# Kernel tuning notes

Hardware: AMD Instinct MI355X
Metric: run time of the kernel (lower is better)

## Reference

```python
import jax, jax.numpy as jnp
import numpy as np

D_K = 1024
D_V = 1024
D_IN = 1024
D_MODEL = 1024
NUM_HEADS = 16


def setup_inputs() -> dict:
    key = jax.random.key(0)
    k1, k2, k3, k4, k5 = jax.random.split(key, 5)
    x = jax.random.normal(k1, (4, 2048, D_IN), dtype=jnp.float32)
    # trunc_normal init approximated by clipped normal
    W_Q = jnp.clip(jax.random.normal(k2, (D_K, D_IN), dtype=jnp.float32), -2.0, 2.0)
    W_K = jnp.clip(jax.random.normal(k3, (D_K, D_IN), dtype=jnp.float32), -2.0, 2.0)
    W_V = jnp.clip(jax.random.normal(k4, (D_V, D_IN), dtype=jnp.float32), -2.0, 2.0)
    W_O = jnp.clip(jax.random.normal(k5, (D_MODEL, D_V), dtype=jnp.float32), -2.0, 2.0)
    return {"x": x, "W_Q": W_Q, "W_K": W_K, "W_V": W_V, "W_O": W_O}


def reference(x, W_Q, W_K, W_V, W_O):
    b, s, _ = x.shape
    h = NUM_HEADS
    hd_k = D_K // h
    hd_v = D_V // h
    wq = W_Q.reshape(h, hd_k, D_IN)
    wk = W_K.reshape(h, hd_k, D_IN)
    wv = W_V.reshape(h, hd_v, D_IN)
    # project: [b, h, s, head_dim]
    q = jnp.einsum('hkd,bsd->bhsk', wq, x)
    k = jnp.einsum('hkd,bsd->bhsk', wk, x)
    v = jnp.einsum('hvd,bsd->bhsv', wv, x)
    scale = 1.0 / jnp.sqrt(jnp.float32(hd_k))
    scores = jnp.einsum('bhnk,bhmk->bhnm', q, k) * scale  # [b,h,s,s]
    causal = jnp.tril(jnp.ones((s, s), dtype=bool))
    scores = jnp.where(causal, scores, -jnp.inf)
    attn = jax.nn.softmax(scores, axis=-1)
    out = jnp.einsum('bhnm,bhmv->bhnv', attn, v)  # [b,h,s,hd_v]
    out = out.transpose(0, 2, 1, 3).reshape(b, s, D_V)  # concat heads
    return jnp.einsum('ov,bsv->bso', W_O, out)
```

## Files before the change

kernel.cpp:

```cpp
#include <hip/hip_runtime.h>
#include <hip/hip_bf16.h>

typedef __bf16 bf16_t;
typedef __bf16 bf16x4 __attribute__((ext_vector_type(4)));
typedef __bf16 bf16x8 __attribute__((ext_vector_type(8)));
typedef float f32x4 __attribute__((ext_vector_type(4)));

#define MFMA16(a, b, c) __builtin_amdgcn_mfma_f32_16x16x32_bf16((a), (b), (c), 0, 0, 0)

#if __has_builtin(__builtin_amdgcn_exp2f)
#define EXP2(x) __builtin_amdgcn_exp2f(x)
#else
#define EXP2(x) exp2f(x)
#endif

__device__ inline void g2l16(const void* g, void* l) {
    __builtin_amdgcn_global_load_lds((const __attribute__((address_space(1))) void*)g,
                                     (__attribute__((address_space(3))) void*)l, 16, 0, 0);
}

__global__ __launch_bounds__(256) void cvt_split_k(const float* __restrict__ src,
                                                   bf16_t* __restrict__ hi,
                                                   bf16_t* __restrict__ lo, int n4) {
    int i = blockIdx.x * 256 + threadIdx.x;
    if (i < n4) {
        float4 v = reinterpret_cast<const float4*>(src)[i];
        bf16x4 h, l;
        float f;
        f = v.x; h[0] = (__bf16)f; l[0] = (__bf16)(f - (float)h[0]);
        f = v.y; h[1] = (__bf16)f; l[1] = (__bf16)(f - (float)h[1]);
        f = v.z; h[2] = (__bf16)f; l[2] = (__bf16)(f - (float)h[2]);
        f = v.w; h[3] = (__bf16)f; l[3] = (__bf16)(f - (float)h[3]);
        reinterpret_cast<bf16x4*>(hi)[i] = h;
        reinterpret_cast<bf16x4*>(lo)[i] = l;
    }
}

__global__ __launch_bounds__(256) void cvt_weights_k(const float* __restrict__ Wq,
                                                     const float* __restrict__ Wk,
                                                     const float* __restrict__ Wv,
                                                     const float* __restrict__ Wo,
                                                     bf16_t* __restrict__ WQKh, bf16_t* __restrict__ WQKl,
                                                     bf16_t* __restrict__ Wvh, bf16_t* __restrict__ Woh) {
    const int i = blockIdx.x * 256 + threadIdx.x;
    const int which = blockIdx.y;
    if (which <= 1) {
        const float c = (which == 0) ? 0.125f * 1.4426950408889634f : 1.0f;
        const int off = which * 262144;
        float4 v = reinterpret_cast<const float4*>(which == 0 ? Wq : Wk)[i];
        bf16x4 h, l;
        float f;
        f = v.x * c; h[0] = (__bf16)f; l[0] = (__bf16)(f - (float)h[0]);
        f = v.y * c; h[1] = (__bf16)f; l[1] = (__bf16)(f - (float)h[1]);
        f = v.z * c; h[2] = (__bf16)f; l[2] = (__bf16)(f - (float)h[2]);
        f = v.w * c; h[3] = (__bf16)f; l[3] = (__bf16)(f - (float)h[3]);
        reinterpret_cast<bf16x4*>(WQKh)[i + off] = h;
        reinterpret_cast<bf16x4*>(WQKl)[i + off] = l;
    } else {
        float4 v = reinterpret_cast<const float4*>(which == 2 ? Wv : Wo)[i];
        bf16x4 o;
        o[0] = (__bf16)v.x; o[1] = (__bf16)v.y; o[2] = (__bf16)v.z; o[3] = (__bf16)v.w;
        reinterpret_cast<bf16x4*>(which == 2 ? Wvh : Woh)[i] = o;
    }
}

template <int LGX>
__device__ inline void xcd_tile(int& bm, int& bn) {
    const int id = blockIdx.y * (1 << LGX) + blockIdx.x;
    const int cpx = ((1 << LGX) * gridDim.y) >> 3;
    const int swz = (id & 7) * cpx + (id >> 3);
    bn = swz & ((1 << LGX) - 1);
    bm = swz >> LGX;
}

template <int MODE>
__global__ __launch_bounds__(256) void gemm_bt(const bf16_t* __restrict__ A,
                                               const bf16_t* __restrict__ B,
                                               void* __restrict__ Cout,
                                               int M, int N, int K) {
    __shared__ __align__(16) bf16_t As[128 * 32];
    __shared__ __align__(16) bf16_t Bs[128 * 32];
    const int tid = threadIdx.x;
    const int w = tid >> 6, lane = tid & 63;
    const int l15 = lane & 15, g = lane >> 4;
    const int wr = w >> 1, wc = w & 1;
    int bm, bn;
    xcd_tile<3>(bm, bn);

    const f32x4 fz = {0.f, 0.f, 0.f, 0.f};
    f32x4 acc[4][4];
#pragma unroll
    for (int m = 0; m < 4; m++)
#pragma unroll
        for (int n = 0; n < 4; n++) acc[m][n] = fz;

    const bf16_t* Ab = A + (size_t)bm * 128 * K;
    const bf16_t* Bb = B + (size_t)bn * 128 * K;
    const int rowL = w * 16 + (lane >> 2);
    const int c8 = (lane & 3) * 8;
    char* AsD = (char*)As + w * 1024;
    char* BsD = (char*)Bs + w * 1024;

    for (int k0 = 0; k0 < K; k0 += 32) {
        g2l16(Ab + (size_t)rowL * K + k0 + c8, AsD);
        g2l16(Ab + (size_t)(rowL + 64) * K + k0 + c8, AsD + 4096);
        g2l16(Bb + (size_t)rowL * K + k0 + c8, BsD);
        g2l16(Bb + (size_t)(rowL + 64) * K + k0 + c8, BsD + 4096);
        __syncthreads();

        bf16x8 af[4], bfr[4];
        const bf16x8* Ap = reinterpret_cast<const bf16x8*>(As + (wr * 64 + l15) * 32 + g * 8);
#pragma unroll
        for (int m = 0; m < 4; m++) af[m] = Ap[m * 64];
        const bf16x8* Bp = reinterpret_cast<const bf16x8*>(Bs + (wc * 64 + l15) * 32 + g * 8);
#pragma unroll
        for (int n = 0; n < 4; n++) bfr[n] = Bp[n * 64];
#pragma unroll
        for (int m = 0; m < 4; m++)
#pragma unroll
            for (int n = 0; n < 4; n++) acc[m][n] = MFMA16(af[m], bfr[n], acc[m][n]);
        __syncthreads();
    }

    if constexpr (MODE == 1) {
        __shared__ __align__(16) bf16_t Ct[128][130];
        const int colL = wc * 64 + l15;
        const int rowB = wr * 64 + g * 4;
#pragma unroll
        for (int m = 0; m < 4; m++)
#pragma unroll
            for (int n = 0; n < 4; n++) {
                bf16x4 c4;
#pragma unroll
                for (int r = 0; r < 4; r++) c4[r] = (__bf16)acc[m][n][r];
                *reinterpret_cast<bf16x4*>(&Ct[colL + n * 16][rowB + m * 16]) = c4;
            }
        __syncthreads();
        const int bb = (bm * 128) >> 11;
        const int s0 = (bm * 128) & 2047;
        const int vg = tid >> 3, scc = tid & 7;
        bf16_t* Vtb = (bf16_t*)Cout + (size_t)bb * 1024 * 2048;
#pragma unroll
        for (int u = 0; u < 4; u++)
#pragma unroll
            for (int hh = 0; hh < 2; hh++) {
                const int v = u * 32 + vg;
                const int s = hh * 64 + scc * 8;
                *reinterpret_cast<int4*>(&Vtb[(size_t)(bn * 128 + v) * 2048 + s0 + s]) =
                    *reinterpret_cast<const int4*>(&Ct[v][s]);
            }
    } else {
        const int row0 = bm * 128 + wr * 64 + g * 4;
        const int col0 = bn * 128 + wc * 64 + l15;
#pragma unroll
        for (int m = 0; m < 4; m++)
#pragma unroll
            for (int n = 0; n < 4; n++)
#pragma unroll
                for (int r = 0; r < 4; r++) {
                    int row = row0 + m * 16 + r;
                    int col = col0 + n * 16;
                    float v = acc[m][n][r];
                    if (MODE == 0) {
                        ((bf16_t*)Cout)[(size_t)row * N + col] = (__bf16)v;
                    } else {
                        ((float*)Cout)[(size_t)row * N + col] = v;
                    }
                }
    }
}

__global__ __launch_bounds__(256) void gemm_splitQK(const bf16_t* __restrict__ Ah,
                                                    const bf16_t* __restrict__ Al,
                                                    const bf16_t* __restrict__ Bh,
                                                    const bf16_t* __restrict__ Bl,
                                                    bf16_t* __restrict__ Qh,
                                                    bf16_t* __restrict__ Ql,
                                                    bf16_t* __restrict__ Kh,
                                                    bf16_t* __restrict__ Kl,
                                                    int K) {
    __shared__ __align__(16) bf16_t Ash[128 * 32];
    __shared__ __align__(16) bf16_t Asl[128 * 32];
    __shared__ __align__(16) bf16_t Bsh[128 * 32];
    __shared__ __align__(16) bf16_t Bsl[128 * 32];
    const int tid = threadIdx.x;
    const int w = tid >> 6, lane = tid & 63;
    const int l15 = lane & 15, g = lane >> 4;
    const int wr = w >> 1, wc = w & 1;
    int bm, bn;
    xcd_tile<4>(bm, bn);

    const f32x4 fz = {0.f, 0.f, 0.f, 0.f};
    f32x4 acc[4][4];
#pragma unroll
    for (int m = 0; m < 4; m++)
#pragma unroll
        for (int n = 0; n < 4; n++) acc[m][n] = fz;

    const size_t aoff = (size_t)bm * 128 * K;
    const size_t boff = (size_t)bn * 128 * K;
    const int rowL = w * 16 + (lane >> 2);
    const int c8 = (lane & 3) * 8;
    const size_t g0 = (size_t)rowL * K + c8;
    const size_t g1 = (size_t)(rowL + 64) * K + c8;

    for (int k0 = 0; k0 < K; k0 += 32) {
        g2l16(Ah + aoff + g0 + k0, (char*)Ash + w * 1024);
        g2l16(Ah + aoff + g1 + k0, (char*)Ash + w * 1024 + 4096);
        g2l16(Al + aoff + g0 + k0, (char*)Asl + w * 1024);
        g2l16(Al + aoff + g1 + k0, (char*)Asl + w * 1024 + 4096);
        g2l16(Bh + boff + g0 + k0, (char*)Bsh + w * 1024);
        g2l16(Bh + boff + g1 + k0, (char*)Bsh + w * 1024 + 4096);
        g2l16(Bl + boff + g0 + k0, (char*)Bsl + w * 1024);
        g2l16(Bl + boff + g1 + k0, (char*)Bsl + w * 1024 + 4096);
        __syncthreads();

        bf16x8 ah[4], al[4], bh[4], bl[4];
        const int ao = (wr * 64 + l15) * 32 + g * 8;
        const int bo = (wc * 64 + l15) * 32 + g * 8;
#pragma unroll
        for (int m = 0; m < 4; m++) {
            ah[m] = *reinterpret_cast<const bf16x8*>(Ash + ao + m * 512);
            al[m] = *reinterpret_cast<const bf16x8*>(Asl + ao + m * 512);
        }
#pragma unroll
        for (int n = 0; n < 4; n++) {
            bh[n] = *reinterpret_cast<const bf16x8*>(Bsh + bo + n * 512);
            bl[n] = *reinterpret_cast<const bf16x8*>(Bsl + bo + n * 512);
        }
#pragma unroll
        for (int m = 0; m < 4; m++)
#pragma unroll
            for (int n = 0; n < 4; n++) {
                acc[m][n] = MFMA16(ah[m], bh[n], acc[m][n]);
                acc[m][n] = MFMA16(al[m], bh[n], acc[m][n]);
                acc[m][n] = MFMA16(ah[m], bl[n], acc[m][n]);
            }
        __syncthreads();
    }

    bf16_t* Ch = (bn < 8) ? Qh : Kh;
    bf16_t* Cl = (bn < 8) ? Ql : Kl;
    const int row0 = bm * 128 + wr * 64 + g * 4;
    const int col0 = (bn * 128 + wc * 64 + l15) & 1023;
#pragma unroll
    for (int m = 0; m < 4; m++)
#pragma unroll
        for (int n = 0; n < 4; n++)
#pragma unroll
            for (int r = 0; r < 4; r++) {
                size_t idx = (size_t)(row0 + m * 16 + r) * 1024 + col0 + n * 16;
                float v = acc[m][n][r];
                bf16_t h = (__bf16)v;
                Ch[idx] = h;
                Cl[idx] = (__bf16)(v - (float)h);
            }
}

__global__ __launch_bounds__(256) void attn_k(const bf16_t* __restrict__ Qh,
                                              const bf16_t* __restrict__ Ql,
                                              const bf16_t* __restrict__ Kh,
                                              const bf16_t* __restrict__ Kl,
                                              const bf16_t* __restrict__ Vt,
                                              bf16_t* __restrict__ Opart,
                                              float* __restrict__ ML) {
    const int L = (int)blockIdx.x + 8 * ((int)blockIdx.y + 16 * (int)blockIdx.z);
    const int px = (L >> 3) & 7;
    const int G = (L & 7) | ((L >> 6) << 3);
    const int h = G & 15;
    const int zz = G >> 4;
    const int b = zz >> 1, hf = zz & 1;
    const int tid = threadIdx.x, w = tid >> 6, lane = tid & 63;
    const int l15 = lane & 15, g = lane >> 4;

    __shared__ __align__(16) bf16_t Ks[4096];
    __shared__ __align__(16) bf16_t Ls[4096];
    __shared__ __align__(16) bf16_t Vs[4096];
    __shared__ __align__(16) bf16_t Ps[4][1024];

    const size_t boff = (size_t)b * 2048 * 1024;
    const size_t vbase = (size_t)b * 1024 * 2048 + (size_t)(h * 64) * 2048;

    const int sr = tid >> 3;
    const int sc = tid & 7;
    const int wo0 = sr * 8 + (sc ^ (sr & 7));
    const int wo1 = wo0 + 256;

    int4 sK0, sK1, sL0, sL1, sV0, sV1;
#define STAGE_LOAD(T)                                                               \
    do {                                                                            \
        const int kv0_ = (T) * 64;                                                  \
        const bf16_t* kp = Kh + boff + (size_t)(kv0_ + sr) * 1024 + h * 64 + sc * 8;\
        const bf16_t* lp = Kl + boff + (size_t)(kv0_ + sr) * 1024 + h * 64 + sc * 8;\
        const bf16_t* vp = Vt + vbase + (size_t)sr * 2048 + kv0_ + sc * 8;          \
        sK0 = *(const int4*)kp; sK1 = *(const int4*)(kp + 32 * 1024);               \
        sL0 = *(const int4*)lp; sL1 = *(const int4*)(lp + 32 * 1024);               \
        sV0 = *(const int4*)vp; sV1 = *(const int4*)(vp + 32 * 2048);               \
    } while (0)
#define STAGE_WRITE()                                                               \
    do {                                                                            \
        ((int4*)Ks)[wo0] = sK0; ((int4*)Ks)[wo1] = sK1;                             \
        ((int4*)Ls)[wo0] = sL0; ((int4*)Ls)[wo1] = sL1;                             \
        ((int4*)Vs)[wo0] = sV0; ((int4*)Vs)[wo1] = sV1;                             \
    } while (0)

    const f32x4 fz = {0.f, 0.f, 0.f, 0.f};
    bf16_t* Op = Opart + (size_t)hf * 8 * 1024 * 1024;
    float* MLp = ML + (size_t)hf * 8192 * 16 * 2;

#pragma unroll 1
    for (int it = 0; it < 2; ++it) {
        const int qt = it ? (15 - px) : px;
        const int qrw = qt * 128 + w * 32;

        bf16x8 qhf[2][2], qlf[2][2];
#pragma unroll
        for (int m = 0; m < 2; m++)
#pragma unroll
            for (int kk = 0; kk < 2; kk++) {
                size_t qi = boff + (size_t)(qrw + m * 16 + l15) * 1024 + h * 64 + kk * 32 + g * 8;
                qhf[m][kk] = *reinterpret_cast<const bf16x8*>(Qh + qi);
                qlf[m][kk] = *reinterpret_cast<const bf16x8*>(Ql + qi);
            }

        f32x4 oacc[2][4];
#pragma unroll
        for (int m = 0; m < 2; m++)
#pragma unroll
            for (int n = 0; n < 4; n++) oacc[m][n] = fz;
        float mst[2] = {-__builtin_inff(), -__builtin_inff()};
        float lst[2] = {0.f, 0.f};

        const int t0 = hf ? qt + 1 : 0;
        const int t1 = hf ? 2 * qt + 1 : qt;
        STAGE_LOAD(t0);
        STAGE_WRITE();
        __syncthreads();

        for (int t = t0; t <= t1; ++t) {
            const int kv0 = t * 64;
            if (t < t1) STAGE_LOAD(t + 1);

            if (kv0 <= qrw + 31) {
                f32x4 st[2][4];
#pragma unroll
                for (int m = 0; m < 2; m++)
#pragma unroll
                    for (int n = 0; n < 4; n++) st[m][n] = fz;
                __builtin_amdgcn_s_setprio(1);
#pragma unroll
                for (int kk = 0; kk < 2; kk++)
#pragma unroll
                    for (int n = 0; n < 4; n++) {
                        const int off = (n * 16 + l15) * 64 + (((kk * 4 + g) ^ (l15 & 7)) << 3);
                        bf16x8 khf = *reinterpret_cast<const bf16x8*>(&Ks[off]);
                        bf16x8 klf = *reinterpret_cast<const bf16x8*>(&Ls[off]);
#pragma unroll
                        for (int m = 0; m < 2; m++) {
                            st[m][n] = MFMA16(khf, qhf[m][kk], st[m][n]);
                            st[m][n] = MFMA16(khf, qlf[m][kk], st[m][n]);
                            st[m][n] = MFMA16(klf, qhf[m][kk], st[m][n]);
                        }
                    }
                __builtin_amdgcn_s_setprio(0);

                const bool diag = (kv0 + 63 > qrw);
#pragma unroll
                for (int m = 0; m < 2; m++) {
                    const int qrow = qrw + m * 16 + l15;
                    float pmax = -__builtin_inff();
                    if (diag) {
                        const int klim = qrow - kv0;
#pragma unroll
                        for (int n = 0; n < 4; n++)
#pragma unroll
                            for (int r = 0; r < 4; r++) {
                                float s = st[m][n][r];
                                if (n * 16 + g * 4 + r > klim) s = -__builtin_inff();
                                st[m][n][r] = s;
                                pmax = fmaxf(pmax, s);
                            }
                    } else {
#pragma unroll
                        for (int n = 0; n < 4; n++)
#pragma unroll
                            for (int r = 0; r < 4; r++) pmax = fmaxf(pmax, st[m][n][r]);
                    }
                    pmax = fmaxf(pmax, __shfl_xor(pmax, 16));
                    pmax = fmaxf(pmax, __shfl_xor(pmax, 32));
                    const float mn = fmaxf(mst[m], pmax);
                    const float alpha = EXP2(mst[m] - mn);
                    mst[m] = mn;
                    float rs = 0.f;
#pragma unroll
                    for (int n = 0; n < 4; n++)
#pragma unroll
                        for (int r = 0; r < 4; r++) {
                            float pe = EXP2(st[m][n][r] - mn);
                            st[m][n][r] = pe;
                            rs += pe;
                        }
                    rs += __shfl_xor(rs, 16);
                    rs += __shfl_xor(rs, 32);
                    lst[m] = lst[m] * alpha + rs;
#pragma unroll
                    for (int n = 0; n < 4; n++) oacc[m][n] *= alpha;

#pragma unroll
                    for (int n = 0; n < 4; n++) {
                        bf16x4 p4;
#pragma unroll
                        for (int r = 0; r < 4; r++) p4[r] = (__bf16)st[m][n][r];
                        const int chunk = (2 * n + (g >> 1)) ^ (l15 & 7);
                        *reinterpret_cast<bf16x4*>(&Ps[w][l15 * 64 + chunk * 8 + (g & 1) * 4]) = p4;
                    }

                    asm volatile("s_waitcnt lgkmcnt(0)" ::: "memory");
                    __builtin_amdgcn_sched_barrier(0);

                    __builtin_amdgcn_s_setprio(1);
#pragma unroll
                    for (int kk = 0; kk < 2; kk++) {
                        bf16x8 pa = *reinterpret_cast<const bf16x8*>(
                            &Ps[w][l15 * 64 + (((kk * 4 + g) ^ (l15 & 7)) << 3)]);
#pragma unroll
                        for (int n = 0; n < 4; n++) {
                            const int voff = (n * 16 + l15) * 64 + (((kk * 4 + g) ^ (l15 & 7)) << 3);
                            bf16x8 vf = *reinterpret_cast<const bf16x8*>(&Vs[voff]);
                            oacc[m][n] = MFMA16(vf, pa, oacc[m][n]);
                        }
                    }
                    __builtin_amdgcn_s_setprio(0);
                }
            }
            __syncthreads();
            if (t < t1) STAGE_WRITE();
            __syncthreads();
        }

#pragma unroll
        for (int m = 0; m < 2; m++) {
            const int qrow = qrw + m * 16 + l15;
#pragma unroll
            for (int n = 0; n < 4; n++) {
                bf16x4 o4;
#pragma unroll
                for (int r = 0; r < 4; r++) o4[r] = (__bf16)oacc[m][n][r];
                *reinterpret_cast<bf16x4*>(&Op[boff + (size_t)qrow * 1024 + h * 64 + n * 16 + g * 4]) = o4;
            }
            if (g == 0) {
                const int grow = b * 2048 + qrow;
                MLp[(grow * 16 + h) * 2 + 0] = mst[m];
                MLp[(grow * 16 + h) * 2 + 1] = lst[m];
            }
        }
    }
#undef STAGE_LOAD
#undef STAGE_WRITE
}

__global__ __launch_bounds__(256) void attn_combine_k(const bf16_t* __restrict__ Op0,
                                                      const bf16_t* __restrict__ Op1,
                                                      const float* __restrict__ ML,
                                                      bf16_t* __restrict__ O) {
    const int t = blockIdx.x * 256 + threadIdx.x;
    const int row = t >> 7;
    const int h = (t >> 3) & 15;
    const float m1 = ML[(row * 16 + h) * 2 + 0];
    const float l1 = ML[(row * 16 + h) * 2 + 1];
    const float m2 = ML[(8192 * 16 + row * 16 + h) * 2 + 0];
    const float l2 = ML[(8192 * 16 + row * 16 + h) * 2 + 1];
    const float mx = fmaxf(m1, m2);
    float w1 = (l1 > 0.f) ? EXP2(m1 - mx) : 0.f;
    float w2 = (l2 > 0.f) ? EXP2(m2 - mx) : 0.f;
    const float inv = 1.f / (l1 * w1 + l2 * w2);
    w1 *= inv; w2 *= inv;
    bf16x8 a = reinterpret_cast<const bf16x8*>(Op0)[t];
    bf16x8 c = reinterpret_cast<const bf16x8*>(Op1)[t];
    bf16x8 o;
#pragma unroll
    for (int i = 0; i < 8; i++) o[i] = (__bf16)((float)a[i] * w1 + (float)c[i] * w2);
    reinterpret_cast<bf16x8*>(O)[t] = o;
}

extern "C" void kernel_launch(void* const* d_in, const int* in_sizes, int n_in,
                              void* d_out, int out_size, void* d_ws, size_t ws_size,
                              hipStream_t stream) {
    const float* x  = (const float*)d_in[0];
    const float* Wq = (const float*)d_in[1];
    const float* Wk = (const float*)d_in[2];
    const float* Wv = (const float*)d_in[3];
    const float* Wo = (const float*)d_in[4];

    char* ws = (char*)d_ws;
    const size_t MB = (size_t)1 << 20;
    bf16_t* xh   = (bf16_t*)(ws);
    bf16_t* xl   = (bf16_t*)(ws + 16 * MB);
    bf16_t* Qh   = (bf16_t*)(ws + 32 * MB);
    bf16_t* Ql   = (bf16_t*)(ws + 48 * MB);
    bf16_t* Kh   = (bf16_t*)(ws + 64 * MB);
    bf16_t* Kl   = (bf16_t*)(ws + 80 * MB);
    bf16_t* Vt   = (bf16_t*)(ws + 96 * MB);
    bf16_t* Ob   = (bf16_t*)(ws + 112 * MB);
    bf16_t* WQKh = (bf16_t*)(ws + 128 * MB);
    bf16_t* WQKl = (bf16_t*)(ws + 132 * MB);
    bf16_t* Wvh  = (bf16_t*)(ws + 136 * MB);
    bf16_t* Woh  = (bf16_t*)(ws + 138 * MB);
    bf16_t* Opart = (bf16_t*)(ws);
    float*  ML    = (float*)(ws + 128 * MB);

    cvt_split_k<<<8192, 256, 0, stream>>>(x, xh, xl, 2097152);
    cvt_weights_k<<<dim3(1024, 4), 256, 0, stream>>>(Wq, Wk, Wv, Wo,
                                                     WQKh, WQKl, Wvh, Woh);

    gemm_splitQK<<<dim3(16, 64), 256, 0, stream>>>(xh, xl, WQKh, WQKl,
                                                   Qh, Ql, Kh, Kl, 1024);
    gemm_bt<1><<<dim3(8, 64), 256, 0, stream>>>(xh, Wvh, Vt, 8192, 1024, 1024);

    attn_k<<<dim3(8, 16, 8), 256, 0, stream>>>(Qh, Ql, Kh, Kl, Vt, Opart, ML);
    attn_combine_k<<<4096, 256, 0, stream>>>(Opart, Opart + (size_t)8 * 1024 * 1024, ML, Ob);

    gemm_bt<2><<<dim3(8, 64), 256, 0, stream>>>(Ob, Woh, d_out, 8192, 1024, 1024);
}
```

Baseline: 288.6 us.

## Switch attention kernel from 16x16x32 to 32x32x16 MFMA tiles

Rewrites the attention inner loop so each wave handles its 32 query rows with 32x32x16 bf16 MFMAs instead of two 16-row groups of 16x16x32 MFMAs. Each lane now owns one query row, so the softmax row reductions need one cross-lane shuffle instead of two, and the loop over m sub-tiles is gone. LDS fragment indexing, the swizzle, the causal mask mapping, the P staging buffer (doubled in size) and the output store layout are all redone for the new accumulator layout. The intent is fewer MFMA issues, fewer LDS reads per FLOP and less softmax overhead. The cost is larger accumulators (16-wide vectors), which raises register pressure, and larger shared memory use.

```diff
diff --git a/kernel.cpp b/kernel.cpp
--- a/kernel.cpp
+++ b/kernel.cpp
@@ -5,8 +5,10 @@
 typedef __bf16 bf16x4 __attribute__((ext_vector_type(4)));
 typedef __bf16 bf16x8 __attribute__((ext_vector_type(8)));
 typedef float f32x4 __attribute__((ext_vector_type(4)));
+typedef float f32x16 __attribute__((ext_vector_type(16)));
 
 #define MFMA16(a, b, c) __builtin_amdgcn_mfma_f32_16x16x32_bf16((a), (b), (c), 0, 0, 0)
+#define MFMA32(a, b, c) __builtin_amdgcn_mfma_f32_32x32x16_bf16((a), (b), (c), 0, 0, 0)
 
 #if __has_builtin(__builtin_amdgcn_exp2f)
 #define EXP2(x) __builtin_amdgcn_exp2f(x)
@@ -271,12 +273,13 @@
     const int zz = G >> 4;
     const int b = zz >> 1, hf = zz & 1;
     const int tid = threadIdx.x, w = tid >> 6, lane = tid & 63;
-    const int l15 = lane & 15, g = lane >> 4;
+    const int l31 = lane & 31, g5 = lane >> 5;
+    const int key = l31 & 7;
 
     __shared__ __align__(16) bf16_t Ks[4096];
     __shared__ __align__(16) bf16_t Ls[4096];
     __shared__ __align__(16) bf16_t Vs[4096];
-    __shared__ __align__(16) bf16_t Ps[4][1024];
+    __shared__ __align__(16) bf16_t Ps[4][2048];
 
     const size_t boff = (size_t)b * 2048 * 1024;
     const size_t vbase = (size_t)b * 1024 * 2048 + (size_t)(h * 64) * 2048;
@@ -304,7 +307,6 @@
         ((int4*)Vs)[wo0] = sV0; ((int4*)Vs)[wo1] = sV1;                             \
     } while (0)
 
-    const f32x4 fz = {0.f, 0.f, 0.f, 0.f};
     bf16_t* Op = Opart + (size_t)hf * 8 * 1024 * 1024;
     float* MLp = ML + (size_t)hf * 8192 * 16 * 2;
 
@@ -312,24 +314,20 @@
     for (int it = 0; it < 2; ++it) {
         const int qt = it ? (15 - px) : px;
         const int qrw = qt * 128 + w * 32;
-
-        bf16x8 qhf[2][2], qlf[2][2];
-#pragma unroll
-        for (int m = 0; m < 2; m++)
-#pragma unroll
-            for (int kk = 0; kk < 2; kk++) {
-                size_t qi = boff + (size_t)(qrw + m * 16 + l15) * 1024 + h * 64 + kk * 32 + g * 8;
-                qhf[m][kk] = *reinterpret_cast<const bf16x8*>(Qh + qi);
-                qlf[m][kk] = *reinterpret_cast<const bf16x8*>(Ql + qi);
-            }
-
-        f32x4 oacc[2][4];
-#pragma unroll
-        for (int m = 0; m < 2; m++)
-#pragma unroll
-            for (int n = 0; n < 4; n++) oacc[m][n] = fz;
-        float mst[2] = {-__builtin_inff(), -__builtin_inff()};
-        float lst[2] = {0.f, 0.f};
+        const int qrow = qrw + l31;
+
+        bf16x8 qhf[4], qlf[4];
+#pragma unroll
+        for (int kk = 0; kk < 4; kk++) {
+            size_t qi = boff + (size_t)qrow * 1024 + h * 64 + kk * 16 + g5 * 8;
+            qhf[kk] = *reinterpret_cast<const bf16x8*>(Qh + qi);
+            qlf[kk] = *reinterpret_cast<const bf16x8*>(Ql + qi);
+        }
+
+        f32x16 oacc0, oacc1;
+#pragma unroll
+        for (int i = 0; i < 16; i++) { oacc0[i] = 0.f; oacc1[i] = 0.f; }
+        float mst = -__builtin_inff(), lst = 0.f;
 
         const int t0 = hf ? qt + 1 : 0;
         const int t1 = hf ? 2 * qt + 1 : qt;
@@ -342,96 +340,87 @@
             if (t < t1) STAGE_LOAD(t + 1);
 
             if (kv0 <= qrw + 31) {
-                f32x4 st[2][4];
-#pragma unroll
-                for (int m = 0; m < 2; m++)
-#pragma unroll
-                    for (int n = 0; n < 4; n++) st[m][n] = fz;
+                f32x16 st0, st1;
+#pragma unroll
+                for (int i = 0; i < 16; i++) { st0[i] = 0.f; st1[i] = 0.f; }
                 __builtin_amdgcn_s_setprio(1);
 #pragma unroll
-                for (int kk = 0; kk < 2; kk++)
-#pragma unroll
-                    for (int n = 0; n < 4; n++) {
-                        const int off = (n * 16 + l15) * 64 + (((kk * 4 + g) ^ (l15 & 7)) << 3);
-                        bf16x8 khf = *reinterpret_cast<const bf16x8*>(&Ks[off]);
-                        bf16x8 klf = *reinterpret_cast<const bf16x8*>(&Ls[off]);
-#pragma unroll
-                        for (int m = 0; m < 2; m++) {
-                            st[m][n] = MFMA16(khf, qhf[m][kk], st[m][n]);
-                            st[m][n] = MFMA16(khf, qlf[m][kk], st[m][n]);
-                            st[m][n] = MFMA16(klf, qhf[m][kk], st[m][n]);
-                        }
+                for (int kk = 0; kk < 4; kk++) {
+                    const int cs = (((kk << 1) | g5) ^ key) << 3;
+                    bf16x8 kh0 = *reinterpret_cast<const bf16x8*>(&Ks[l31 * 64 + cs]);
+                    bf16x8 kl0 = *reinterpret_cast<const bf16x8*>(&Ls[l31 * 64 + cs]);
+                    bf16x8 kh1 = *reinterpret_cast<const bf16x8*>(&Ks[(l31 + 32) * 64 + cs]);
+                    bf16x8 kl1 = *reinterpret_cast<const bf16x8*>(&Ls[(l31 + 32) * 64 + cs]);
+                    st0 = MFMA32(kh0, qhf[kk], st0);
+                    st0 = MFMA32(kh0, qlf[kk], st0);
+                    st0 = MFMA32(kl0, qhf[kk], st0);
+                    st1 = MFMA32(kh1, qhf[kk], st1);
+                    st1 = MFMA32(kh1, qlf[kk], st1);
+                    st1 = MFMA32(kl1, qhf[kk], st1);
+                }
+                __builtin_amdgcn_s_setprio(0);
+
+                if (kv0 + 63 > qrow) {
+                    const int klim = qrow - kv0;
+#pragma unroll
+                    for (int i = 0; i < 16; i++) {
+                        const int kvl = (i & 3) + 8 * (i >> 2) + 4 * g5;
+                        if (kvl > klim) st0[i] = -__builtin_inff();
+                        if (kvl + 32 > klim) st1[i] = -__builtin_inff();
                     }
+                }
+                float pmax = -__builtin_inff();
+#pragma unroll
+                for (int i = 0; i < 16; i++) {
+                    pmax = fmaxf(pmax, st0[i]);
+                    pmax = fmaxf(pmax, st1[i]);
+                }
+                pmax = fmaxf(pmax, __shfl_xor(pmax, 32));
+                const float mn = fmaxf(mst, pmax);
+                const float alpha = EXP2(mst - mn);
+                mst = mn;
+                float rs = 0.f;
+#pragma unroll
+                for (int i = 0; i < 16; i++) {
+                    float p0 = EXP2(st0[i] - mn);
+                    float p1 = EXP2(st1[i] - mn);
+                    st0[i] = p0;
+                    st1[i] = p1;
+                    rs += p0 + p1;
+                }
+                rs += __shfl_xor(rs, 32);
+                lst = lst * alpha + rs;
+#pragma unroll
+                for (int i = 0; i < 16; i++) { oacc0[i] *= alpha; oacc1[i] *= alpha; }
+
+#pragma unroll
+                for (int qd = 0; qd < 4; qd++) {
+                    bf16x4 p4a, p4b;
+#pragma unroll
+                    for (int r = 0; r < 4; r++) {
+                        p4a[r] = (__bf16)st0[4 * qd + r];
+                        p4b[r] = (__bf16)st1[4 * qd + r];
+                    }
+                    const int ca = (qd ^ key) << 3;
+                    const int cb = ((4 + qd) ^ key) << 3;
+                    *reinterpret_cast<bf16x4*>(&Ps[w][l31 * 64 + ca + 4 * g5]) = p4a;
+                    *reinterpret_cast<bf16x4*>(&Ps[w][l31 * 64 + cb + 4 * g5]) = p4b;
+                }
+
+                asm volatile("s_waitcnt lgkmcnt(0)" ::: "memory");
+                __builtin_amdgcn_sched_barrier(0);
+
+                __builtin_amdgcn_s_setprio(1);
+#pragma unroll
+                for (int kks = 0; kks < 4; kks++) {
+                    const int cs = (((kks << 1) | g5) ^ key) << 3;
+                    bf16x8 pa = *reinterpret_cast<const bf16x8*>(&Ps[w][l31 * 64 + cs]);
+                    bf16x8 vf0 = *reinterpret_cast<const bf16x8*>(&Vs[l31 * 64 + cs]);
+                    bf16x8 vf1 = *reinterpret_cast<const bf16x8*>(&Vs[(l31 + 32) * 64 + cs]);
+                    oacc0 = MFMA32(vf0, pa, oacc0);
+                    oacc1 = MFMA32(vf1, pa, oacc1);
+                }
                 __builtin_amdgcn_s_setprio(0);
-
-                const bool diag = (kv0 + 63 > qrw);
-#pragma unroll
-                for (int m = 0; m < 2; m++) {
-                    const int qrow = qrw + m * 16 + l15;
-                    float pmax = -__builtin_inff();
-                    if (diag) {
-                        const int klim = qrow - kv0;
-#pragma unroll
-                        for (int n = 0; n < 4; n++)
-#pragma unroll
-                            for (int r = 0; r < 4; r++) {
-                                float s = st[m][n][r];
-                                if (n * 16 + g * 4 + r > klim) s = -__builtin_inff();
-                                st[m][n][r] = s;
-                                pmax = fmaxf(pmax, s);
-                            }
-                    } else {
-#pragma unroll
-                        for (int n = 0; n < 4; n++)
-#pragma unroll
-                            for (int r = 0; r < 4; r++) pmax = fmaxf(pmax, st[m][n][r]);
-                    }
-                    pmax = fmaxf(pmax, __shfl_xor(pmax, 16));
-                    pmax = fmaxf(pmax, __shfl_xor(pmax, 32));
-                    const float mn = fmaxf(mst[m], pmax);
-                    const float alpha = EXP2(mst[m] - mn);
-                    mst[m] = mn;
-                    float rs = 0.f;
-#pragma unroll
-                    for (int n = 0; n < 4; n++)
-#pragma unroll
-                        for (int r = 0; r < 4; r++) {
-                            float pe = EXP2(st[m][n][r] - mn);
-                            st[m][n][r] = pe;
-                            rs += pe;
-                        }
-                    rs += __shfl_xor(rs, 16);
-                    rs += __shfl_xor(rs, 32);
-                    lst[m] = lst[m] * alpha + rs;
-#pragma unroll
-                    for (int n = 0; n < 4; n++) oacc[m][n] *= alpha;
-
-#pragma unroll
-                    for (int n = 0; n < 4; n++) {
-                        bf16x4 p4;
-#pragma unroll
-                        for (int r = 0; r < 4; r++) p4[r] = (__bf16)st[m][n][r];
-                        const int chunk = (2 * n + (g >> 1)) ^ (l15 & 7);
-                        *reinterpret_cast<bf16x4*>(&Ps[w][l15 * 64 + chunk * 8 + (g & 1) * 4]) = p4;
-                    }
-
-                    asm volatile("s_waitcnt lgkmcnt(0)" ::: "memory");
-                    __builtin_amdgcn_sched_barrier(0);
-
-                    __builtin_amdgcn_s_setprio(1);
-#pragma unroll
-                    for (int kk = 0; kk < 2; kk++) {
-                        bf16x8 pa = *reinterpret_cast<const bf16x8*>(
-                            &Ps[w][l15 * 64 + (((kk * 4 + g) ^ (l15 & 7)) << 3)]);
-#pragma unroll
-                        for (int n = 0; n < 4; n++) {
-                            const int voff = (n * 16 + l15) * 64 + (((kk * 4 + g) ^ (l15 & 7)) << 3);
-                            bf16x8 vf = *reinterpret_cast<const bf16x8*>(&Vs[voff]);
-                            oacc[m][n] = MFMA16(vf, pa, oacc[m][n]);
-                        }
-                    }
-                    __builtin_amdgcn_s_setprio(0);
-                }
             }
             __syncthreads();
             if (t < t1) STAGE_WRITE();
@@ -439,20 +428,21 @@
         }
 
 #pragma unroll
-        for (int m = 0; m < 2; m++) {
-            const int qrow = qrw + m * 16 + l15;
-#pragma unroll
-            for (int n = 0; n < 4; n++) {
-                bf16x4 o4;
-#pragma unroll
-                for (int r = 0; r < 4; r++) o4[r] = (__bf16)oacc[m][n][r];
-                *reinterpret_cast<bf16x4*>(&Op[boff + (size_t)qrow * 1024 + h * 64 + n * 16 + g * 4]) = o4;
+        for (int qd = 0; qd < 4; qd++) {
+            bf16x4 o4a, o4b;
+#pragma unroll
+            for (int r = 0; r < 4; r++) {
+                o4a[r] = (__bf16)oacc0[4 * qd + r];
+                o4b[r] = (__bf16)oacc1[4 * qd + r];
             }
-            if (g == 0) {
-                const int grow = b * 2048 + qrow;
-                MLp[(grow * 16 + h) * 2 + 0] = mst[m];
-                MLp[(grow * 16 + h) * 2 + 1] = lst[m];
-            }
+            const size_t base = boff + (size_t)qrow * 1024 + h * 64 + 8 * qd + 4 * g5;
+            *reinterpret_cast<bf16x4*>(&Op[base]) = o4a;
+            *reinterpret_cast<bf16x4*>(&Op[base + 32]) = o4b;
+        }
+        if (g5 == 0) {
+            const int grow = b * 2048 + qrow;
+            MLp[(grow * 16 + h) * 2 + 0] = mst;
+            MLp[(grow * 16 + h) * 2 + 1] = lst;
         }
     }
 #undef STAGE_LOAD
```

Measured after the change: 327.5 us. 1.13x slower.
